# Performance work log

Measured on AMD Instinct MI355X. Metric: run time of the kernel, lower is better.

Reference implementation:

```python
import jax, jax.numpy as jnp
import numpy as np

T, B, E, H = 64, 64, 128, 256
N_ITEMS, N_DATA = 50000, 20000
EPS = 1e-8


def setup_inputs() -> dict:
    key = jax.random.key(0)
    ks = jax.random.split(key, 20)
    lengths = jnp.sort(jax.random.randint(ks[0], (B,), 1, T + 1))[::-1]
    lengths = lengths.at[0].set(T)  # pack_padded_sequence expects max length first
    x = jax.random.randint(ks[1], (T, B), 1, N_ITEMS)
    tmask = jnp.arange(T)[:, None] < lengths[None, :]
    x = jnp.where(tmask, x, 0)  # padding index 0
    s = 0.05
    emb_table = (jax.random.normal(ks[2], (N_ITEMS, E)) * s).at[0].set(0.0)  # padding_idx=0
    data_embeddings = jax.random.normal(ks[3], (N_DATA, E)) * s
    return {
        'x': x, 'lengths': lengths,
        'emb_table': emb_table, 'data_embeddings': data_embeddings,
        'W_ih': jax.random.normal(ks[4], (4 * H, E)) * s,
        'W_hh': jax.random.normal(ks[5], (4 * H, H)) * s,
        'b_ih': jax.random.normal(ks[6], (4 * H,)) * s,
        'b_hh': jax.random.normal(ks[7], (4 * H,)) * s,
        'Wq': jax.random.normal(ks[8], (H, H)) * s, 'bq': jax.random.normal(ks[9], (H,)) * s,
        'Wk': jax.random.normal(ks[10], (H, H)) * s, 'bk': jax.random.normal(ks[11], (H,)) * s,
        'Wv': jax.random.normal(ks[12], (H, H)) * s, 'bv': jax.random.normal(ks[13], (H,)) * s,
        'W_out': jax.random.normal(ks[14], (E, H)) * s, 'b_out': jax.random.normal(ks[15], (E,)) * s,
    }


def _forward(x, lengths, emb_table, data_embeddings, W_ih, W_hh, b_ih, b_hh,
             Wq, bq, Wk, bk, Wv, bv, W_out, b_out):
    t_len, b_sz = x.shape
    e_dim = emb_table.shape[1]
    h_dim = W_hh.shape[1]

    embs0 = emb_table[x]  # (T, B, E); dropout is identity in eval mode
    initial_embs = jax.lax.stop_gradient(embs0)  # .clone().detach() in original

    # PositionalEncoding: original slices by x.size(1) == batch dim (faithful quirk)
    pos = jnp.arange(b_sz, dtype=jnp.float32)[:, None]
    div = jnp.exp(jnp.arange(0, e_dim, 2, dtype=jnp.float32) * (-jnp.log(10000.0) / e_dim))
    enc = jnp.stack([jnp.sin(pos * div), jnp.cos(pos * div)], axis=-1).reshape(b_sz, e_dim)
    embs = embs0 + enc[None, :, :]  # broadcast over time

    # single-layer LSTM over time (gate order i, f, g, o)
    def step(carry, x_t):
        h, c = carry
        gates = x_t @ W_ih.T + h @ W_hh.T + (b_ih + b_hh)  # (B, 4H)
        i, f, g, o = jnp.split(gates, 4, axis=-1)
        c = jax.nn.sigmoid(f) * c + jax.nn.sigmoid(i) * jnp.tanh(g)
        h = jax.nn.sigmoid(o) * jnp.tanh(c)
        return (h, c), h

    h0 = jnp.zeros((b_sz, h_dim), embs.dtype)
    (_, _), lstm_out = jax.lax.scan(step, (h0, h0), embs)  # (T, B, H)

    # pack/pad round-trip zeroes outputs past each length (LSTM is causal)
    tmask = jnp.arange(t_len)[:, None] < lengths[None, :]  # (T, B)
    lstm_out = lstm_out * tmask[:, :, None]
    lstm_out = lstm_out.transpose(1, 0, 2)  # (B, T, H)

    padding_mask = jnp.sum(lstm_out, axis=-1) != 0  # (B, T)

    q = lstm_out @ Wq.T + bq
    k = lstm_out @ Wk.T + bk
    v = lstm_out @ Wv.T + bv
    score = jnp.einsum('bth,bsh->bts', q, k) / jnp.sqrt(jnp.float32(h_dim))
    score = jnp.where(padding_mask[:, None, :], score, -jnp.inf)
    attn = jax.nn.softmax(score, axis=2)
    weighted = jnp.einsum('bts,bsh->bth', attn, v)  # (B, T, H)
    attn_output = jnp.mean(weighted, axis=1) @ W_out.T + b_out  # (B, E)

    # kNN: fused normalize + matmul + argmin + gather over all T at once
    qn = initial_embs / jnp.clip(jnp.linalg.norm(initial_embs, axis=-1, keepdims=True), EPS)
    dn = data_embeddings / jnp.clip(jnp.linalg.norm(data_embeddings, axis=-1, keepdims=True), EPS)
    sims = jnp.einsum('tbe,ne->tbn', qn, dn)  # (T, B, N_DATA)
    idx = jnp.argmax(sims, axis=-1)  # argmin of (1 - sim)
    closest = jnp.mean(data_embeddings[idx], axis=0)  # (B, E)

    attn_output = attn_output * closest
    return attn_output @ emb_table.T  # (B, n_items)


def reference(x, lengths, emb_table, data_embeddings, W_ih, W_hh, b_ih, b_hh,
              Wq, bq, Wk, bk, Wv, bv, W_out, b_out):
    return _forward(x, lengths, emb_table, data_embeddings, W_ih, W_hh, b_ih, b_hh,
                    Wq, bq, Wk, bk, Wv, bv, W_out, b_out)
```

## Files before the change

### kernel.cpp

```cpp
#include <hip/hip_runtime.h>

typedef unsigned int uint;
typedef unsigned short ushort;
typedef unsigned long long u64;

#define NITEMS 50000
#define NDATA  20000
#define BLKCAP 4096u
#define OVCAP  65536u

#define OFF_LSTMOUT   0x0000000ULL
#define OFF_HX        0x0400000ULL
#define OFF_PACKED    0x0440000ULL
#define OFF_PACKED2   0x0448000ULL
#define OFF_HITCNTS   0x0450000ULL
#define OFF_OHITCNT   0x0450800ULL
#define MEMSET_BYTES  0x0451000ULL
#define OFF_QMARGIN   0x0451000ULL
#define OFF_XW        0x0560000ULL
#define OFF_QKV       0x1560000ULL
#define OFF_HITBUF    OFF_QKV
#define OFF_WIHT      0x2160000ULL
#define OFF_WQKVT     0x21E0000ULL
#define OFF_BIASIH    0x22A0000ULL
#define OFF_BQKV      0x22A1000ULL
#define OFF_DNSCALE   0x22A2000ULL
#define OFF_CLOSEST   0x22B6000ULL
#define OFF_AV        0x22BE000ULL
#define OFF_DEMB16    0x22C6000ULL
#define OFF_A16       0x27A8000ULL

__device__ __forceinline__ ushort f2bf(float f) {
  union { float f; uint u; } v; v.f = f;
  uint u = v.u;
  return (ushort)((u + 0x7FFFu + ((u >> 16) & 1u)) >> 16);
}
__device__ __forceinline__ uint fkey(float f) {
  union { float f; uint u; } v; v.f = f;
  return (v.u & 0x80000000u) ? ~v.u : (v.u | 0x80000000u);
}
__device__ __forceinline__ u64 shfl_xor_u64(u64 v, int off) {
  uint lo = (uint)v, hi = (uint)(v >> 32);
  lo = (uint)__shfl_xor((int)lo, off);
  hi = (uint)__shfl_xor((int)hi, off);
  return ((u64)hi << 32) | (u64)lo;
}

typedef __attribute__((ext_vector_type(8))) short short8;
typedef __attribute__((ext_vector_type(4))) float floatx4;

#define R32(M) M(0) M(1) M(2) M(3) M(4) M(5) M(6) M(7) M(8) M(9) M(10) M(11) \
  M(12) M(13) M(14) M(15) M(16) M(17) M(18) M(19) M(20) M(21) M(22) M(23) \
  M(24) M(25) M(26) M(27) M(28) M(29) M(30) M(31)

__global__ __launch_bounds__(256) void prep_kernel(
    const int* __restrict__ x,
    const float* __restrict__ emb, const float* __restrict__ demb,
    const float* __restrict__ W_ih,
    const float* __restrict__ Wq, const float* __restrict__ Wk, const float* __restrict__ Wv,
    const float* __restrict__ b_ih, const float* __restrict__ b_hh,
    const float* __restrict__ bq, const float* __restrict__ bk, const float* __restrict__ bv,
    float* __restrict__ dnscale, ushort* __restrict__ demb16, ushort* __restrict__ a16,
    float* __restrict__ wiht, float* __restrict__ wqkvt,
    float* __restrict__ biasih, float* __restrict__ bqkv,
    float* __restrict__ qmargin, u64* __restrict__ packed2)
{
  int blk = blockIdx.x, tid = threadIdx.x;
  if (blk < 5000) {
    int row = blk * 4 + (tid >> 6);
    int lane = tid & 63;
    float2 d = *(const float2*)(demb + (size_t)row * 128 + lane * 2);
    float s = d.x * d.x + d.y * d.y;
    for (int off = 32; off; off >>= 1) s += __shfl_xor(s, off);
    if (lane == 0) dnscale[row] = 1.0f / fmaxf(sqrtf(s), 1e-8f);
  } else if (blk < 6250) {
    size_t base = ((size_t)(blk - 5000) * 256 + tid) * 8;
    float4 f1 = *(const float4*)(demb + base);
    float4 f2 = *(const float4*)(demb + base + 4);
    uint4 o;
    o.x = (uint)f2bf(f1.x) | ((uint)f2bf(f1.y) << 16);
    o.y = (uint)f2bf(f1.z) | ((uint)f2bf(f1.w) << 16);
    o.z = (uint)f2bf(f2.x) | ((uint)f2bf(f2.y) << 16);
    o.w = (uint)f2bf(f2.z) | ((uint)f2bf(f2.w) << 16);
    *(uint4*)(demb16 + base) = o;
  } else if (blk < 6506) {
    int idx = (blk - 6250) * 256 + tid;
    int m = idx >> 4, seg = idx & 15;
    const float* src = emb + (size_t)x[m] * 128 + seg * 8;
    float4 f1 = *(const float4*)(src);
    float4 f2 = *(const float4*)(src + 4);
    uint4 o;
    o.x = (uint)f2bf(f1.x) | ((uint)f2bf(f1.y) << 16);
    o.y = (uint)f2bf(f1.z) | ((uint)f2bf(f1.w) << 16);
    o.z = (uint)f2bf(f2.x) | ((uint)f2bf(f2.y) << 16);
    o.w = (uint)f2bf(f2.z) | ((uint)f2bf(f2.w) << 16);
    *(uint4*)(a16 + (size_t)m * 128 + seg * 8) = o;
  } else if (blk < 7018) {
    int f = (blk - 6506) * 256 + tid;
    int r = f >> 7, e = f & 127;
    wiht[e * 1024 + r] = W_ih[f];
  } else if (blk < 7786) {
    int f = (blk - 7018) * 256 + tid;
    int w = f >> 16; int rem = f & 65535;
    int r = rem >> 8, e = rem & 255;
    const float* src = (w == 0) ? Wq : (w == 1) ? Wk : Wv;
    wqkvt[e * 768 + w * 256 + r] = src[rem];
  } else if (blk < 7790) {
    int idx = (blk - 7786) * 256 + tid;
    if (idx < 1024) biasih[idx] = b_ih[idx] + b_hh[idx];
  } else if (blk < 7793) {
    int idx = (blk - 7790) * 256 + tid;
    if (idx < 768) {
      int w = idx >> 8; int r = idx & 255;
      const float* src = (w == 0) ? bq : (w == 1) ? bk : bv;
      bqkv[idx] = src[r];
    }
  } else {
    int row = (blk - 7793) * 4 + (tid >> 6);
    int lane = tid & 63;
    float2 d = *(const float2*)(emb + (size_t)x[row] * 128 + lane * 2);
    float s = d.x * d.x + d.y * d.y;
    for (int off = 32; off; off >>= 1) s += __shfl_xor(s, off);
    if (lane == 0) {
      if (s == 0.f) {
        qmargin[row] = -1e30f;
        packed2[row] = ((u64)fkey(0.0f) << 32) | 0xFFFFFFFFull;
      } else {
        qmargin[row] = 0.017f * sqrtf(s) + 1e-5f;
      }
    }
  }
}

__global__ __launch_bounds__(256) void xw_kernel(
    const int* __restrict__ x, const float* __restrict__ emb,
    const float* __restrict__ wiht, const float* __restrict__ biasih,
    float* __restrict__ xW)
{
  __shared__ __align__(16) float At[128 * 16];
  int blk = blockIdx.x, tid = threadIdx.x;
  int m0 = blk * 16;
  for (int c = 0; c < 8; ++c) {
    int idx = c * 256 + tid;
    int mm = idx >> 7, e = idx & 127;
    int m = m0 + mm;
    int bcol = m & 63;
    int xv = x[m];
    float val = emb[(size_t)xv * 128 + e];
    int j = e >> 1;
    float arg = (float)bcol * __expf((float)j * -0.14391157f);
    val += (e & 1) ? cosf(arg) : sinf(arg);
    At[e * 16 + mm] = val;
  }
  __syncthreads();
  int quad = tid >> 6, l = tid & 63;
  for (int rp = 0; rp < 4; ++rp) {
    int r = rp * 256 + l * 4;
    float acc[4][4] = {};
    for (int e = 0; e < 128; ++e) {
      float4 wv4 = *(const float4*)(wiht + e * 1024 + r);
      float4 av4 = *(const float4*)(At + e * 16 + quad * 4);
      float am[4] = {av4.x, av4.y, av4.z, av4.w};
      float wr4[4] = {wv4.x, wv4.y, wv4.z, wv4.w};
      #pragma unroll
      for (int mi = 0; mi < 4; ++mi)
        #pragma unroll
        for (int ri = 0; ri < 4; ++ri)
          acc[mi][ri] += am[mi] * wr4[ri];
    }
    float4 bv4 = *(const float4*)(biasih + r);
    #pragma unroll
    for (int mi = 0; mi < 4; ++mi) {
      size_t m = (size_t)(m0 + quad * 4 + mi);
      float4 o;
      o.x = acc[mi][0] + bv4.x; o.y = acc[mi][1] + bv4.y;
      o.z = acc[mi][2] + bv4.z; o.w = acc[mi][3] + bv4.w;
      *(float4*)(xW + m * 1024 + r) = o;
    }
  }
}

__global__ __launch_bounds__(256) void knn_kernel(
    const ushort* __restrict__ a16, const ushort* __restrict__ demb16,
    const float* __restrict__ dnscale, const float* __restrict__ qmargin,
    u64* __restrict__ packed, uint* __restrict__ hitcnts, uint* __restrict__ ohitcnt,
    uint* __restrict__ hitbuf)
{
  __shared__ __align__(16) ushort b_sh[2][64 * 144];
  __shared__ uint lcnt;
  int blk = blockIdx.x, tid = threadIdx.x;
  int chunk = blk & 15, mt = blk >> 4;
  int wv = tid >> 6, lane = tid & 63;
  int col = lane & 15, quad = lane >> 4;
  int M0 = mt * 128;
  if (tid == 0) lcnt = 0;
  short8 afrag[2][4];
  #pragma unroll
  for (int s = 0; s < 2; ++s) {
    int mrow = M0 + s * 64 + wv * 16 + col;
    #pragma unroll
    for (int kf = 0; kf < 4; ++kf)
      afrag[s][kf] = *(const short8*)(a16 + (size_t)mrow * 128 + kf * 32 + quad * 8);
  }
  float best[2][4] = {{-1e30f,-1e30f,-1e30f,-1e30f},{-1e30f,-1e30f,-1e30f,-1e30f}};
  int bidx[2][4] = {};
  int nbase = chunk * 1250, nend = nbase + 1250;
  const int niter = 20;
  int srow = tid >> 4, sseg = tid & 15;
  uint4 stg[4]; float scr[4];

  #pragma unroll
  for (int p = 0; p < 4; ++p) {
    int n = nbase + p * 16 + srow;
    uint4 v = {0u,0u,0u,0u};
    if (n < nend) v = *(const uint4*)(demb16 + (size_t)n * 128 + sseg * 8);
    stg[p] = v;
  }
  #pragma unroll
  for (int ns = 0; ns < 4; ++ns) {
    int n = nbase + ns * 16 + col;
    scr[ns] = (n < nend) ? dnscale[n] : 0.f;
  }
  for (int it = 0; it < niter; ++it) {
    int n0 = nbase + it * 64;
    ushort* bsh = b_sh[it & 1];
    #pragma unroll
    for (int p = 0; p < 4; ++p)
      *(uint4*)(&bsh[(p * 16 + srow) * 144 + sseg * 8]) = stg[p];
    float mysc[4] = {scr[0], scr[1], scr[2], scr[3]};
    __syncthreads();
    if (it + 1 < niter) {
      int nb = n0 + 64;
      #pragma unroll
      for (int p = 0; p < 4; ++p) {
        int n = nb + p * 16 + srow;
        uint4 v = {0u,0u,0u,0u};
        if (n < nend) v = *(const uint4*)(demb16 + (size_t)n * 128 + sseg * 8);
        stg[p] = v;
      }
      #pragma unroll
      for (int ns = 0; ns < 4; ++ns) {
        int n = nb + ns * 16 + col;
        scr[ns] = (n < nend) ? dnscale[n] : 0.f;
      }
    }
    #pragma unroll
    for (int ns = 0; ns < 4; ++ns) {
      short8 bfr[4];
      #pragma unroll
      for (int kf = 0; kf < 4; ++kf)
        bfr[kf] = *(const short8*)(&bsh[(ns * 16 + col) * 144 + kf * 32 + quad * 8]);
      int n = n0 + ns * 16 + col;
      float sc = mysc[ns];
      bool valid = (n < nend);
      #pragma unroll
      for (int s = 0; s < 2; ++s) {
        floatx4 acc = {0.f, 0.f, 0.f, 0.f};
        #pragma unroll
        for (int kf = 0; kf < 4; ++kf)
          acc = __builtin_amdgcn_mfma_f32_16x16x32_bf16(afrag[s][kf], bfr[kf], acc, 0, 0, 0);
        #pragma unroll
        for (int r = 0; r < 4; ++r) {
          float sim = acc[r] * sc;
          if (valid && sim > best[s][r]) { best[s][r] = sim; bidx[s][r] = n; }
        }
      }
    }
  }
  float thr[2][4];
  #pragma unroll
  for (int s = 0; s < 2; ++s)
    #pragma unroll
    for (int r = 0; r < 4; ++r) {
      u64 p = ((u64)fkey(best[s][r]) << 32) | (u64)(0xFFFFFFFFu - (uint)bidx[s][r]);
      #pragma unroll
      for (int off = 1; off < 16; off <<= 1) {
        u64 o = shfl_xor_u64(p, off);
        if (o > p) p = o;
      }
      int m = M0 + s * 64 + wv * 16 + quad * 4 + r;
      union { uint u; float f; } bu;
      uint k = (uint)(p >> 32);
      bu.u = (k & 0x80000000u) ? (k & 0x7FFFFFFFu) : ~k;
      thr[s][r] = bu.f - qmargin[m];
      if (col == 0)
        atomicMax((unsigned long long*)&packed[m], (unsigned long long)p);
    }
  __syncthreads();

  uint* myregion = hitbuf + (size_t)blk * BLKCAP;
  uint* ovregion = hitbuf + (size_t)512 * BLKCAP;
  #pragma unroll
  for (int p = 0; p < 4; ++p) {
    int n = nbase + p * 16 + srow;
    uint4 v = {0u,0u,0u,0u};
    if (n < nend) v = *(const uint4*)(demb16 + (size_t)n * 128 + sseg * 8);
    stg[p] = v;
  }
  #pragma unroll
  for (int ns = 0; ns < 4; ++ns) {
    int n = nbase + ns * 16 + col;
    scr[ns] = (n < nend) ? dnscale[n] : 0.f;
  }
  for (int it = 0; it < niter; ++it) {
    int n0 = nbase + it * 64;
    ushort* bsh = b_sh[it & 1];
    #pragma unroll
    for (int p = 0; p < 4; ++p)
      *(uint4*)(&bsh[(p * 16 + srow) * 144 + sseg * 8]) = stg[p];
    float mysc[4] = {scr[0], scr[1], scr[2], scr[3]};
    __syncthreads();
    if (it + 1 < niter) {
      int nb = n0 + 64;
      #pragma unroll
      for (int p = 0; p < 4; ++p) {
        int n = nb + p * 16 + srow;
        uint4 v = {0u,0u,0u,0u};
        if (n < nend) v = *(const uint4*)(demb16 + (size_t)n * 128 + sseg * 8);
        stg[p] = v;
      }
      #pragma unroll
      for (int ns = 0; ns < 4; ++ns) {
        int n = nb + ns * 16 + col;
        scr[ns] = (n < nend) ? dnscale[n] : 0.f;
      }
    }
    #pragma unroll
    for (int ns = 0; ns < 4; ++ns) {
      short8 bfr[4];
      #pragma unroll
      for (int kf = 0; kf < 4; ++kf)
        bfr[kf] = *(const short8*)(&bsh[(ns * 16 + col) * 144 + kf * 32 + quad * 8]);
      int n = n0 + ns * 16 + col;
      float sc = mysc[ns];
      bool valid = (n < nend);
      #pragma unroll
      for (int s = 0; s < 2; ++s) {
        floatx4 acc = {0.f, 0.f, 0.f, 0.f};
        #pragma unroll
        for (int kf = 0; kf < 4; ++kf)
          acc = __builtin_amdgcn_mfma_f32_16x16x32_bf16(afrag[s][kf], bfr[kf], acc, 0, 0, 0);
        #pragma unroll
        for (int r = 0; r < 4; ++r) {
          float sim = acc[r] * sc;
          bool hit = valid && (sim >= thr[s][r]);
          u64 mask = __ballot(hit);
          if (mask) {
            uint lcntv = (uint)__popcll(mask);
            int leader = __ffsll((unsigned long long)mask) - 1;
            uint base = 0;
            if (lane == leader) base = atomicAdd(&lcnt, lcntv);
            base = (uint)__shfl((int)base, leader);
            if (hit) {
              uint pos = base + (uint)__popcll(mask & ((1ull << lane) - 1ull));
              uint mm = (uint)(M0 + s * 64 + wv * 16 + quad * 4 + r);
              uint rec = (mm << 15) | (uint)n;
              if (pos < BLKCAP) {
                myregion[pos] = rec;
              } else {
                uint op = atomicAdd(ohitcnt, 1u);
                if (op < OVCAP) ovregion[op] = rec;
              }
            }
          }
        }
      }
    }
  }
  __syncthreads();
  if (tid == 0) hitcnts[blk] = lcnt;
}

__global__ __launch_bounds__(256) void rescore_kernel(
    const uint* __restrict__ hitbuf, const uint* __restrict__ hitcnts,
    const uint* __restrict__ ohitcnt, const u64* __restrict__ packed,
    const int* __restrict__ x, const float* __restrict__ emb,
    const float* __restrict__ demb, const float* __restrict__ dnscale,
    u64* __restrict__ packed2)
{
  int blk = blockIdx.x, tid = threadIdx.x;
  uint gid = blk * 256 + tid;
  if (gid < 4096) {
    uint m = gid;
    uint n = 0xFFFFFFFFu - (uint)(packed[m] & 0xFFFFFFFFull);
    if (n < NDATA) {
      const float* q = emb + (size_t)x[m] * 128;
      const float* d = demb + (size_t)n * 128;
      double p = 0.0;
      #pragma unroll 8
      for (int e = 0; e < 128; e += 2) {
        float2 qv = *(const float2*)(q + e);
        float2 dv = *(const float2*)(d + e);
        p += (double)qv.x * (double)dv.x + (double)qv.y * (double)dv.y;
      }
      float sx = (float)(p * (double)dnscale[n]);
      u64 key = ((u64)fkey(sx) << 32) | (u64)(0xFFFFFFFFu - n);
      atomicMax((unsigned long long*)&packed2[m], (unsigned long long)key);
    }
  }
  const uint* src; uint cnt; uint stride;
  if (blk < 512) {
    src = hitbuf + (size_t)blk * BLKCAP;
    cnt = hitcnts[blk]; if (cnt > BLKCAP) cnt = BLKCAP;
    stride = 256;
  } else {
    src = hitbuf + (size_t)512 * BLKCAP + (blk - 512) * 256 + 0;
    src = hitbuf + (size_t)512 * BLKCAP;
    cnt = *ohitcnt; if (cnt > OVCAP) cnt = OVCAP;
    stride = 16 * 256;
  }
  uint start = (blk < 512) ? tid : (uint)((blk - 512) * 256 + tid);
  for (uint h = start; h < cnt; h += stride) {
    uint rec = src[h];
    uint m = rec >> 15, n = rec & 0x7FFFu;
    if (m >= 4096 || n >= NDATA) continue;
    const float* q = emb + (size_t)x[m] * 128;
    const float* d = demb + (size_t)n * 128;
    double p = 0.0;
    #pragma unroll 8
    for (int e = 0; e < 128; e += 2) {
      float2 qv = *(const float2*)(q + e);
      float2 dv = *(const float2*)(d + e);
      p += (double)qv.x * (double)dv.x + (double)qv.y * (double)dv.y;
    }
    float sx = (float)(p * (double)dnscale[n]);
    u64 key = ((u64)fkey(sx) << 32) | (u64)(0xFFFFFFFFu - n);
    atomicMax((unsigned long long*)&packed2[m], (unsigned long long)key);
  }
}

__global__ __launch_bounds__(512, 2) void lstm_kernel(
    const int* __restrict__ lengths, const float* __restrict__ Whh,
    const float* __restrict__ xW, float* __restrict__ lstm_out,
    u64* __restrict__ hx)
{
  __shared__ __align__(16) float h_sh[256];
  __shared__ float part_sh[512];
  int blk = blockIdx.x, tid = threadIdx.x;
  int b = blk & 63, q = blk >> 6;
  int row_local = tid >> 1, half = tid & 1;
  int gate = row_local >> 6, jloc = row_local & 63;
  int grow = gate * 256 + q * 64 + jloc;
  const float4* wp4 = (const float4*)(Whh + (size_t)grow * 256 + half * 128);
#define WDECL(i) float4 tt##i = wp4[i]; \
  float w##i##x = tt##i.x, w##i##y = tt##i.y, w##i##z = tt##i.z, w##i##w = tt##i.w;
  R32(WDECL)
#define WPIN(i) asm volatile("" : "+v"(w##i##x), "+v"(w##i##y), "+v"(w##i##z), "+v"(w##i##w));
  R32(WPIN)
  int len = lengths[b];
  if (tid < 256) h_sh[tid] = 0.f;
  float cval = 0.f;
  int jr = (tid < q * 64) ? tid : tid + 64;
  __syncthreads();
  for (int t = 0; t < len; ++t) {
    if (t > 0) {
      if (tid < 192) {
        u64* slot = hx + (((size_t)(t & 1) * 64 + b) * 256 + jr);
        u64 v = 0; int guard = 0;
        while (true) {
          v = __hip_atomic_load(slot, __ATOMIC_RELAXED, __HIP_MEMORY_SCOPE_AGENT);
          if ((uint)v == (uint)t || ++guard > (1 << 22)) break;
          __builtin_amdgcn_s_sleep(1);
        }
        union { uint u; float f; } cv; cv.u = (uint)(v >> 32);
        h_sh[jr] = cv.f;
      }
      __syncthreads();
    }
    const float4* h4 = (const float4*)(h_sh + half * 128);
    float acc = 0.f;
#define WACC(i) { float4 hv = h4[i]; \
    acc += w##i##x * hv.x + w##i##y * hv.y + w##i##z * hv.z + w##i##w * hv.w; }
    R32(WACC)
    part_sh[tid] = acc;
    __syncthreads();
    if (tid < 64) {
      const float* xwrow = xW + ((size_t)t * 64 + b) * 1024 + q * 64 + tid;
      float gi = part_sh[tid * 2]         + part_sh[tid * 2 + 1]         + xwrow[0];
      float gf = part_sh[(64 + tid) * 2]  + part_sh[(64 + tid) * 2 + 1]  + xwrow[256];
      float gg = part_sh[(128 + tid) * 2] + part_sh[(128 + tid) * 2 + 1] + xwrow[512];
      float go = part_sh[(192 + tid) * 2] + part_sh[(192 + tid) * 2 + 1] + xwrow[768];
      float ii = 1.f / (1.f + __expf(-gi));
      float ff = 1.f / (1.f + __expf(-gf));
      float oo = 1.f / (1.f + __expf(-go));
      cval = ff * cval + ii * tanhf(gg);
      float hv = oo * tanhf(cval);
      int j = q * 64 + tid;
      lstm_out[((size_t)b * 64 + t) * 256 + j] = hv;
      h_sh[j] = hv;
      union { float f; uint u; } cu; cu.f = hv;
      u64 pk = ((u64)cu.u << 32) | (u64)(uint)(t + 1);
      __hip_atomic_store(hx + (((size_t)((t + 1) & 1) * 64 + b) * 256 + j), pk,
                         __ATOMIC_RELAXED, __HIP_MEMORY_SCOPE_AGENT);
    }
    __syncthreads();
  }
}

__global__ __launch_bounds__(128) void closest_kernel(
    const u64* __restrict__ packed2, const float* __restrict__ demb,
    float* __restrict__ closest)
{
  int b = blockIdx.x, tid = threadIdx.x;
  float s = 0.f;
  for (int t = 0; t < 64; ++t) {
    uint low = (uint)(packed2[t * 64 + b] & 0xFFFFFFFFull);
    uint n = 0xFFFFFFFFu - low;
    if (n >= NDATA) n = 0;
    s += demb[(size_t)n * 128 + tid];
  }
  closest[b * 128 + tid] = s * (1.0f / 64.0f);
}

__global__ __launch_bounds__(256) void qkv_kernel(
    const float* __restrict__ lstm_out, const float* __restrict__ wqkvt,
    const float* __restrict__ bqkv, float* __restrict__ qkv)
{
  __shared__ __align__(16) float At[256 * 16];
  int blk = blockIdx.x, tid = threadIdx.x;
  int m0 = blk * 16;
  for (int c = 0; c < 16; ++c)
    At[tid * 16 + c] = lstm_out[((size_t)m0 + c) * 256 + tid];
  __syncthreads();
  int quad = tid >> 6, l = tid & 63;
  for (int rp = 0; rp < 3; ++rp) {
    int r = rp * 256 + l * 4;
    float acc[4][4] = {};
    for (int e = 0; e < 256; ++e) {
      float4 wv4 = *(const float4*)(wqkvt + (size_t)e * 768 + r);
      float4 av4 = *(const float4*)(At + e * 16 + quad * 4);
      float am[4] = {av4.x, av4.y, av4.z, av4.w};
      float wr4[4] = {wv4.x, wv4.y, wv4.z, wv4.w};
      #pragma unroll
      for (int mi = 0; mi < 4; ++mi)
        #pragma unroll
        for (int ri = 0; ri < 4; ++ri)
          acc[mi][ri] += am[mi] * wr4[ri];
    }
    float4 bv4 = *(const float4*)(bqkv + r);
    #pragma unroll
    for (int mi = 0; mi < 4; ++mi) {
      size_t m = (size_t)(m0 + quad * 4 + mi);
      float4 o;
      o.x = acc[mi][0] + bv4.x; o.y = acc[mi][1] + bv4.y;
      o.z = acc[mi][2] + bv4.z; o.w = acc[mi][3] + bv4.w;
      *(float4*)(qkv + m * 768 + r) = o;
    }
  }
}

__global__ __launch_bounds__(256) void attn_kernel(
    const float* __restrict__ qkv, const int* __restrict__ lengths,
    const float* __restrict__ closest, const float* __restrict__ W_out,
    const float* __restrict__ b_out, float* __restrict__ av)
{
  __shared__ float k_sh[64 * 257];
  __shared__ __align__(16) float q_sh[4 * 256];
  __shared__ float wpart[4 * 64];
  __shared__ float wtot[64];
  __shared__ float out_sh[256];
  int b = blockIdx.x, tid = threadIdx.x;
  int wv = tid >> 6, lane = tid & 63;
  int len = lengths[b];
  for (int s = 0; s < 64; ++s)
    k_sh[s * 257 + tid] = qkv[((size_t)b * 64 + s) * 768 + 256 + tid];
  wpart[tid] = 0.f;
  for (int tq = 0; tq < 16; ++tq) {
    __syncthreads();
    #pragma unroll
    for (int c = 0; c < 4; ++c)
      q_sh[c * 256 + tid] = qkv[((size_t)b * 64 + tq * 4 + c) * 768 + tid];
    __syncthreads();
    const float* krow = k_sh + lane * 257;
    const float* qrow = q_sh + wv * 256;
    float sc = 0.f;
    #pragma unroll 8
    for (int h = 0; h < 256; ++h)
      sc += qrow[h] * krow[h];
    sc *= 0.0625f;
    bool vs = (lane < len);
    float scm = vs ? sc : -1e30f;
    float mx = scm;
    for (int off = 32; off; off >>= 1) mx = fmaxf(mx, __shfl_xor(mx, off));
    float e = vs ? __expf(sc - mx) : 0.f;
    float sum = e;
    for (int off = 32; off; off >>= 1) sum += __shfl_xor(sum, off);
    wpart[wv * 64 + lane] += e / sum;
  }
  __syncthreads();
  if (tid < 64)
    wtot[tid] = (wpart[tid] + wpart[64 + tid] + wpart[128 + tid] + wpart[192 + tid]) * (1.0f / 64.0f);
  __syncthreads();
  {
    float acc = 0.f;
    for (int s = 0; s < 64; ++s)
      acc += wtot[s] * qkv[((size_t)b * 64 + s) * 768 + 512 + tid];
    out_sh[tid] = acc;
  }
  __syncthreads();
  if (tid < 128) {
    const float4* wr = (const float4*)(W_out + (size_t)tid * 256);
    float p = b_out[tid];
    #pragma unroll
    for (int c = 0; c < 64; ++c) {
      float4 u = wr[c];
      p += out_sh[c * 4 + 0] * u.x + out_sh[c * 4 + 1] * u.y
         + out_sh[c * 4 + 2] * u.z + out_sh[c * 4 + 3] * u.w;
    }
    av[tid * 64 + b] = p * closest[b * 128 + tid];
  }
}

__global__ __launch_bounds__(256) void final_kernel(
    const float* __restrict__ emb, const float* __restrict__ av,
    float* __restrict__ out)
{
  int i = blockIdx.x * 256 + threadIdx.x;
  if (i >= NITEMS) return;
  const float4* row = (const float4*)(emb + (size_t)i * 128);
  float acc[64];
  #pragma unroll
  for (int bb = 0; bb < 64; ++bb) acc[bb] = 0.f;
  for (int e4 = 0; e4 < 32; ++e4) {
    float4 u = row[e4];
    float wvv[4] = {u.x, u.y, u.z, u.w};
    const float* ab = av + e4 * 4 * 64;
    #pragma unroll
    for (int j = 0; j < 4; ++j) {
      #pragma unroll
      for (int bb = 0; bb < 64; ++bb)
        acc[bb] += wvv[j] * ab[j * 64 + bb];
    }
  }
  #pragma unroll
  for (int bb = 0; bb < 64; ++bb)
    out[(size_t)bb * NITEMS + i] = acc[bb];
}

extern "C" void kernel_launch(void* const* d_in, const int* in_sizes, int n_in,
                              void* d_out, int out_size, void* d_ws, size_t ws_size,
                              hipStream_t stream)
{
  const int*   x       = (const int*)d_in[0];
  const int*   lengths = (const int*)d_in[1];
  const float* emb     = (const float*)d_in[2];
  const float* demb    = (const float*)d_in[3];
  const float* W_ih    = (const float*)d_in[4];
  const float* W_hh    = (const float*)d_in[5];
  const float* b_ih    = (const float*)d_in[6];
  const float* b_hh    = (const float*)d_in[7];
  const float* Wq      = (const float*)d_in[8];
  const float* bq      = (const float*)d_in[9];
  const float* Wk      = (const float*)d_in[10];
  const float* bk      = (const float*)d_in[11];
  const float* Wv      = (const float*)d_in[12];
  const float* bv      = (const float*)d_in[13];
  const float* W_out   = (const float*)d_in[14];
  const float* b_out   = (const float*)d_in[15];

  char* ws = (char*)d_ws;
  float*  lstm_out = (float*)(ws + OFF_LSTMOUT);
  u64*    hx       = (u64*)(ws + OFF_HX);
  u64*    packed   = (u64*)(ws + OFF_PACKED);
  u64*    packed2  = (u64*)(ws + OFF_PACKED2);
  uint*   hitcnts  = (uint*)(ws + OFF_HITCNTS);
  uint*   ohitcnt  = (uint*)(ws + OFF_OHITCNT);
  float*  qmargin  = (float*)(ws + OFF_QMARGIN);
  uint*   hitbuf   = (uint*)(ws + OFF_HITBUF);
  float*  xW       = (float*)(ws + OFF_XW);
  float*  qkv      = (float*)(ws + OFF_QKV);
  float*  wiht     = (float*)(ws + OFF_WIHT);
  float*  wqkvt    = (float*)(ws + OFF_WQKVT);
  float*  biasih   = (float*)(ws + OFF_BIASIH);
  float*  bqkv     = (float*)(ws + OFF_BQKV);
  float*  dnscale  = (float*)(ws + OFF_DNSCALE);
  float*  closest  = (float*)(ws + OFF_CLOSEST);
  float*  av       = (float*)(ws + OFF_AV);
  ushort* demb16   = (ushort*)(ws + OFF_DEMB16);
  ushort* a16      = (ushort*)(ws + OFF_A16);

  hipMemsetAsync(d_ws, 0, (size_t)MEMSET_BYTES, stream);

  hipLaunchKernelGGL(prep_kernel, dim3(8817), dim3(256), 0, stream,
                     x, emb, demb, W_ih, Wq, Wk, Wv, b_ih, b_hh, bq, bk, bv,
                     dnscale, demb16, a16, wiht, wqkvt, biasih, bqkv,
                     qmargin, packed2);
  hipLaunchKernelGGL(xw_kernel, dim3(256), dim3(256), 0, stream,
                     x, emb, wiht, biasih, xW);
  hipLaunchKernelGGL(knn_kernel, dim3(512), dim3(256), 0, stream,
                     a16, demb16, dnscale, qmargin, packed, hitcnts, ohitcnt, hitbuf);
  hipLaunchKernelGGL(rescore_kernel, dim3(528), dim3(256), 0, stream,
                     hitbuf, hitcnts, ohitcnt, packed, x, emb, demb, dnscale, packed2);
  hipLaunchKernelGGL(lstm_kernel, dim3(256), dim3(512), 0, stream,
                     lengths, W_hh, xW, lstm_out, hx);
  hipLaunchKernelGGL(closest_kernel, dim3(64), dim3(128), 0, stream,
                     packed2, demb, closest);
  hipLaunchKernelGGL(qkv_kernel, dim3(256), dim3(256), 0, stream,
                     lstm_out, wqkvt, bqkv, qkv);
  hipLaunchKernelGGL(attn_kernel, dim3(64), dim3(256), 0, stream,
                     qkv, lengths, closest, W_out, b_out, av);
  hipLaunchKernelGGL(final_kernel, dim3(196), dim3(256), 0, stream,
                     emb, av, (float*)d_out);
}
```

Measured before the change: 632.1 us.

## Restructure LSTM cross-block handoff with mirrored hidden-state buffer and fast polling

The LSTM step loop now publishes each new hidden value to a second mirror buffer via raw global stores, and separate waves (tid>=320) poll that mirror with cache-bypassing loads right after the gate update instead of at the top of the next step. If fast polling fails they fall back to the atomic poll. It also prefetches xW before the matvec, reduces the two half-row partials with a shuffle instead of shared memory, and replaces tanhf with an exp-based formula. The aim is to shorten the per-timestep cross-block synchronization latency that dominates the sequential LSTM. The trade-offs are reliance on inline-asm memory semantics for visibility and slightly different tanh rounding.

```diff
diff --git a/kernel.cpp b/kernel.cpp
--- a/kernel.cpp
+++ b/kernel.cpp
@@ -11,24 +11,25 @@
 
 #define OFF_LSTMOUT   0x0000000ULL
 #define OFF_HX        0x0400000ULL
-#define OFF_PACKED    0x0440000ULL
-#define OFF_PACKED2   0x0448000ULL
-#define OFF_HITCNTS   0x0450000ULL
-#define OFF_OHITCNT   0x0450800ULL
-#define MEMSET_BYTES  0x0451000ULL
-#define OFF_QMARGIN   0x0451000ULL
-#define OFF_XW        0x0560000ULL
-#define OFF_QKV       0x1560000ULL
+#define OFF_HXM       0x0440000ULL
+#define OFF_PACKED    0x0480000ULL
+#define OFF_PACKED2   0x0488000ULL
+#define OFF_HITCNTS   0x0490000ULL
+#define OFF_OHITCNT   0x0490800ULL
+#define MEMSET_BYTES  0x0491000ULL
+#define OFF_QMARGIN   0x0491000ULL
+#define OFF_XW        0x05A0000ULL
+#define OFF_QKV       0x15A0000ULL
 #define OFF_HITBUF    OFF_QKV
-#define OFF_WIHT      0x2160000ULL
-#define OFF_WQKVT     0x21E0000ULL
-#define OFF_BIASIH    0x22A0000ULL
-#define OFF_BQKV      0x22A1000ULL
-#define OFF_DNSCALE   0x22A2000ULL
-#define OFF_CLOSEST   0x22B6000ULL
-#define OFF_AV        0x22BE000ULL
-#define OFF_DEMB16    0x22C6000ULL
-#define OFF_A16       0x27A8000ULL
+#define OFF_WIHT      0x21A0000ULL
+#define OFF_WQKVT     0x2220000ULL
+#define OFF_BIASIH    0x22E0000ULL
+#define OFF_BQKV      0x22E1000ULL
+#define OFF_DNSCALE   0x22E2000ULL
+#define OFF_CLOSEST   0x22F6000ULL
+#define OFF_AV        0x22FE000ULL
+#define OFF_DEMB16    0x2306000ULL
+#define OFF_A16       0x27E8000ULL
 
 __device__ __forceinline__ ushort f2bf(float f) {
   union { float f; uint u; } v; v.f = f;
@@ -404,7 +405,6 @@
     cnt = hitcnts[blk]; if (cnt > BLKCAP) cnt = BLKCAP;
     stride = 256;
   } else {
-    src = hitbuf + (size_t)512 * BLKCAP + (blk - 512) * 256 + 0;
     src = hitbuf + (size_t)512 * BLKCAP;
     cnt = *ohitcnt; if (cnt > OVCAP) cnt = OVCAP;
     stride = 16 * 256;
@@ -432,10 +432,10 @@
 __global__ __launch_bounds__(512, 2) void lstm_kernel(
     const int* __restrict__ lengths, const float* __restrict__ Whh,
     const float* __restrict__ xW, float* __restrict__ lstm_out,
-    u64* __restrict__ hx)
+    u64* __restrict__ hx, u64* __restrict__ hxm)
 {
   __shared__ __align__(16) float h_sh[256];
-  __shared__ float part_sh[512];
+  __shared__ float part_sh[256];
   int blk = blockIdx.x, tid = threadIdx.x;
   int b = blk & 63, q = blk >> 6;
   int row_local = tid >> 1, half = tid & 1;
@@ -450,48 +450,70 @@
   int len = lengths[b];
   if (tid < 256) h_sh[tid] = 0.f;
   float cval = 0.f;
-  int jr = (tid < q * 64) ? tid : tid + 64;
+  int prm = tid - 320;
+  int jr = (prm < q * 64) ? prm : prm + 64;
+  bool fast_ok = true;
   __syncthreads();
   for (int t = 0; t < len; ++t) {
-    if (t > 0) {
-      if (tid < 192) {
-        u64* slot = hx + (((size_t)(t & 1) * 64 + b) * 256 + jr);
-        u64 v = 0; int guard = 0;
-        while (true) {
-          v = __hip_atomic_load(slot, __ATOMIC_RELAXED, __HIP_MEMORY_SCOPE_AGENT);
-          if ((uint)v == (uint)t || ++guard > (1 << 22)) break;
-          __builtin_amdgcn_s_sleep(1);
-        }
-        union { uint u; float f; } cv; cv.u = (uint)(v >> 32);
-        h_sh[jr] = cv.f;
-      }
-      __syncthreads();
+    float xw0, xw1, xw2, xw3;
+    if (tid < 64) {
+      const float* xwrow = xW + ((size_t)t * 64 + b) * 1024 + q * 64 + tid;
+      xw0 = xwrow[0]; xw1 = xwrow[256]; xw2 = xwrow[512]; xw3 = xwrow[768];
     }
     const float4* h4 = (const float4*)(h_sh + half * 128);
     float acc = 0.f;
 #define WACC(i) { float4 hv = h4[i]; \
     acc += w##i##x * hv.x + w##i##y * hv.y + w##i##z * hv.z + w##i##w * hv.w; }
     R32(WACC)
-    part_sh[tid] = acc;
+    acc += __shfl_xor(acc, 1);
+    if (!half) part_sh[row_local] = acc;
     __syncthreads();
     if (tid < 64) {
-      const float* xwrow = xW + ((size_t)t * 64 + b) * 1024 + q * 64 + tid;
-      float gi = part_sh[tid * 2]         + part_sh[tid * 2 + 1]         + xwrow[0];
-      float gf = part_sh[(64 + tid) * 2]  + part_sh[(64 + tid) * 2 + 1]  + xwrow[256];
-      float gg = part_sh[(128 + tid) * 2] + part_sh[(128 + tid) * 2 + 1] + xwrow[512];
-      float go = part_sh[(192 + tid) * 2] + part_sh[(192 + tid) * 2 + 1] + xwrow[768];
+      float gi = part_sh[tid]       + xw0;
+      float gf = part_sh[64 + tid]  + xw1;
+      float gg = part_sh[128 + tid] + xw2;
+      float go = part_sh[192 + tid] + xw3;
       float ii = 1.f / (1.f + __expf(-gi));
       float ff = 1.f / (1.f + __expf(-gf));
       float oo = 1.f / (1.f + __expf(-go));
-      cval = ff * cval + ii * tanhf(gg);
-      float hv = oo * tanhf(cval);
+      float tg = 1.f - 2.f / (1.f + __expf(2.f * gg));
+      cval = ff * cval + ii * tg;
+      float tc = 1.f - 2.f / (1.f + __expf(2.f * cval));
+      float hv = oo * tc;
       int j = q * 64 + tid;
-      lstm_out[((size_t)b * 64 + t) * 256 + j] = hv;
-      h_sh[j] = hv;
       union { float f; uint u; } cu; cu.f = hv;
       u64 pk = ((u64)cu.u << 32) | (u64)(uint)(t + 1);
-      __hip_atomic_store(hx + (((size_t)((t + 1) & 1) * 64 + b) * 256 + j), pk,
-                         __ATOMIC_RELAXED, __HIP_MEMORY_SCOPE_AGENT);
+      size_t slot = ((size_t)((t + 1) & 1) * 64 + b) * 256 + j;
+      asm volatile("global_store_dwordx2 %0, %1, off"
+                   :: "v"(hxm + slot), "v"(pk) : "memory");
+      __hip_atomic_store(hx + slot, pk, __ATOMIC_RELAXED, __HIP_MEMORY_SCOPE_AGENT);
+      h_sh[j] = hv;
+      lstm_out[((size_t)b * 64 + t) * 256 + j] = hv;
+    } else if (tid >= 320 && t + 1 < len) {
+      size_t slot = ((size_t)((t + 1) & 1) * 64 + b) * 256 + jr;
+      uint want = (uint)(t + 1);
+      u64 v = 0;
+      bool got = false;
+      if (fast_ok) {
+        const u64* ms = hxm + slot;
+        for (int tries = 0; tries < 32; ++tries) {
+          asm volatile("global_load_dwordx2 %0, %1, off sc0\n\t"
+                       "s_waitcnt vmcnt(0)"
+                       : "=&v"(v) : "v"(ms) : "memory");
+          if ((uint)v == want) { got = true; break; }
+        }
+        if (!got && t > 0) fast_ok = false;
+      }
+      if (!got) {
+        const u64* as = hx + slot;
+        int guard = 0;
+        while (true) {
+          v = __hip_atomic_load(as, __ATOMIC_RELAXED, __HIP_MEMORY_SCOPE_AGENT);
+          if ((uint)v == want || ++guard > (1 << 22)) break;
+        }
+      }
+      union { uint u; float f; } cv; cv.u = (uint)(v >> 32);
+      h_sh[jr] = cv.f;
     }
     __syncthreads();
   }
@@ -661,6 +683,7 @@
   char* ws = (char*)d_ws;
   float*  lstm_out = (float*)(ws + OFF_LSTMOUT);
   u64*    hx       = (u64*)(ws + OFF_HX);
+  u64*    hxm      = (u64*)(ws + OFF_HXM);
   u64*    packed   = (u64*)(ws + OFF_PACKED);
   u64*    packed2  = (u64*)(ws + OFF_PACKED2);
   uint*   hitcnts  = (uint*)(ws + OFF_HITCNTS);
@@ -692,7 +715,7 @@
   hipLaunchKernelGGL(rescore_kernel, dim3(528), dim3(256), 0, stream,
                      hitbuf, hitcnts, ohitcnt, packed, x, emb, demb, dnscale, packed2);
   hipLaunchKernelGGL(lstm_kernel, dim3(256), dim3(512), 0, stream,
-                     lengths, W_hh, xW, lstm_out, hx);
+                     lengths, W_hh, xW, lstm_out, hx, hxm);
   hipLaunchKernelGGL(closest_kernel, dim3(64), dim3(128), 0, stream,
                      packed2, demb, closest);
   hipLaunchKernelGGL(qkv_kernel, dim3(256), dim3(256), 0, stream,
```

After: 609.7 us. 3.5% less time.
